# Performance work log

Hardware: AMD Instinct MI355X
Metric: run time of the kernel (lower is better)

## Reference

```python
import jax, jax.numpy as jnp
import numpy as np

B_SZ, SEQ_LEN, STATE_DIM, D_IN, D_OUT, KX = 8, 2048, 1024, 512, 512, 10


def setup_inputs() -> dict:
    key = jax.random.key(0)
    ks = jax.random.split(key, 7)
    inputs = jax.random.normal(ks[0], (B_SZ, SEQ_LEN, D_IN), dtype=jnp.float32)
    h0 = jax.random.normal(ks[1], (STATE_DIM,), dtype=jnp.float32)
    # exponential_decay_init(lam=15): x = clamp(-1/lam * log(1-u), max=1); A = (1-x)*sign
    u = jax.random.uniform(ks[2], (STATE_DIM,), dtype=jnp.float32)
    x = jnp.minimum(-(1.0 / 15.0) * jnp.log1p(-u), 1.0)
    sign = jnp.sign(jax.random.normal(ks[3], (STATE_DIM,), dtype=jnp.float32))
    A = (1.0 - x) * sign
    Bm = jax.random.normal(ks[4], (D_IN, STATE_DIM), dtype=jnp.float32) / D_IN
    C = jax.random.normal(ks[5], (STATE_DIM, D_OUT), dtype=jnp.float32) / STATE_DIM
    M = jax.random.normal(ks[6], (D_OUT, D_IN, KX), dtype=jnp.float32) / D_OUT
    return {"inputs": inputs, "h0": h0, "A": A, "B": Bm, "C": C, "M": M}


def _ar_preds(M, x):
    # Equivalent to einsum('oik,bli->bklo') + per-k roll + triu mask + sum over k:
    # ar[b,l,:] = sum_{i=0}^{k-1, i<=l} M[:,:,i] @ x[b, l-i, :]
    b, l, d_in = x.shape
    kx = M.shape[2]
    ar = jnp.einsum('oi,bli->blo', M[:, :, 0], x)
    for i in range(1, kx):
        x_shift = jnp.pad(x, ((0, 0), (i, 0), (0, 0)))[:, :l]  # shift right, zero-fill
        ar = ar + jnp.einsum('oi,bli->blo', M[:, :, i], x_shift)
    return ar


def reference(inputs, h0, A, B, C, M):
    b, l, d_in = inputs.shape
    state_dim = A.shape[0]
    # Project inputs once: u_t @ B for all t -> [b, l, s]
    uB = jnp.einsum('bli,is->bls', inputs, B)

    def step(h, u_t):
        h = A * h + u_t  # diagonal recurrence
        return h, h

    h_init = jnp.broadcast_to(h0, (b, state_dim))
    _, hs = jax.lax.scan(step, h_init, jnp.swapaxes(uB, 0, 1))  # [l, b, s]
    hs = jnp.swapaxes(hs, 0, 1)  # [b, l, s]
    lds_out = hs @ C  # [b, l, d_out]
    return lds_out + _ar_preds(M, inputs)
```

## Files before the change

kernel.cpp:

```cpp
#include <hip/hip_runtime.h>

#define B_SZ   8
#define SEQ    2048
#define PSEQ   (SEQ+16)
#define SDIM   1024
#define DIN    512
#define DOUT   512
#define KX     10
#define RTOT   (B_SZ*SEQ)
#define LC     64
#define NC     (SEQ/LC)

typedef __attribute__((ext_vector_type(8))) short short8;
typedef __attribute__((ext_vector_type(4))) float f32x4;
typedef __attribute__((ext_vector_type(4))) unsigned short bfx4;

#define OFF_XP   0UL
#define OFF_UB   16973824UL
#define OFF_HS   50528256UL
#define OFF_BT   84082688UL
#define OFF_CT   85131264UL
#define OFF_MT   86179840UL

__device__ __forceinline__ short f2bf(float f) {
  unsigned u = __builtin_bit_cast(unsigned, f);
  u += 0x7fffu + ((u >> 16) & 1u);
  return (short)(u >> 16);
}
__device__ __forceinline__ float bf2f(unsigned short b) {
  return __builtin_bit_cast(float, (unsigned)b << 16);
}

#define GLOAD16(gp, lp) __builtin_amdgcn_global_load_lds( \
    (const __attribute__((address_space(1))) void*)(gp), \
    (__attribute__((address_space(3))) void*)(lp), 16, 0, 0)
#define WAITVM(n) asm volatile("s_waitcnt vmcnt(" #n ")" ::: "memory")
#define LGKM0()   do { asm volatile("s_waitcnt lgkmcnt(0)" ::: "memory"); \
                       __builtin_amdgcn_sched_barrier(0); } while (0)
#define SBAR() __builtin_amdgcn_s_barrier()

__global__ void k_conv_x(const float* __restrict__ in, short* __restrict__ out) {
  const int NG = RTOT * (DIN / 8);
  for (int g = blockIdx.x * 256 + threadIdx.x; g < NG; g += 2048 * 256) {
    int r = g >> 6, c8 = g & 63;
    int b = r >> 11, t = r & 2047;
    const float4* p = reinterpret_cast<const float4*>(in) + (size_t)g * 2;
    float4 f0 = p[0], f1 = p[1];
    short8 o;
    o[0]=f2bf(f0.x); o[1]=f2bf(f0.y); o[2]=f2bf(f0.z); o[3]=f2bf(f0.w);
    o[4]=f2bf(f1.x); o[5]=f2bf(f1.y); o[6]=f2bf(f1.z); o[7]=f2bf(f1.w);
    *reinterpret_cast<short8*>(out + ((size_t)(b * PSEQ + 16 + t) * DIN + c8 * 8)) = o;
  }
}

__global__ void k_zero_pad(short* __restrict__ Xp) {
  int idx = blockIdx.x * 256 + threadIdx.x;
  if (idx >= B_SZ * 16 * (DIN / 8)) return;
  int b = idx >> 10, rem = idx & 1023;
  int row16 = rem >> 6, c8 = rem & 63;
  const short8 z = {0,0,0,0,0,0,0,0};
  *reinterpret_cast<short8*>(Xp + ((size_t)(b * PSEQ + row16) * DIN + c8 * 8)) = z;
}

__global__ void k_transpose_bf16(const float* __restrict__ in, short* __restrict__ out,
                                 int rows, int cols) {
  __shared__ float t[32][33];
  int bx = blockIdx.x * 32, by = blockIdx.y * 32;
  int tx = threadIdx.x & 31, ty = threadIdx.x >> 5;
  #pragma unroll
  for (int j = 0; j < 32; j += 8)
    t[ty + j][tx] = in[(size_t)(by + ty + j) * cols + (bx + tx)];
  __syncthreads();
  #pragma unroll
  for (int j = 0; j < 32; j += 8)
    out[(size_t)(bx + ty + j) * rows + (by + tx)] = f2bf(t[tx][ty + j]);
}

__global__ void k_prep_M(const float* __restrict__ M, short* __restrict__ Mt) {
  int idx = blockIdx.x * 256 + threadIdx.x;
  if (idx >= DOUT * DIN) return;
  int o = idx / DIN, i = idx - o * DIN;
  const float* src = M + ((size_t)o * DIN + i) * KX;
  #pragma unroll
  for (int t = 0; t < KX; ++t)
    Mt[((size_t)t * DOUT + o) * DIN + i] = f2bf(src[t]);
}

__global__ void k_scan_E(const short* __restrict__ uB, const float* __restrict__ A,
                         float* __restrict__ E) {
  int blk = blockIdx.x, tid = threadIdx.x;
  int b = blk >> 5, c = blk & 31;
  int s0 = tid * 4;
  const short* base = uB + ((size_t)b * SEQ + (size_t)c * LC) * SDIM + s0;
  float a[4], h[4];
  #pragma unroll
  for (int j = 0; j < 4; ++j) { a[j] = A[s0 + j]; h[j] = 0.f; }
  for (int t = 0; t < LC; ++t) {
    bfx4 v = *reinterpret_cast<const bfx4*>(base + (size_t)t * SDIM);
    #pragma unroll
    for (int j = 0; j < 4; ++j) h[j] = fmaf(a[j], h[j], bf2f(v[j]));
  }
  float* ep = E + (size_t)blk * SDIM + s0;
  #pragma unroll
  for (int j = 0; j < 4; ++j) ep[j] = h[j];
}

__global__ void k_scan_S(const float* __restrict__ E, const float* __restrict__ A,
                         const float* __restrict__ h0, float* __restrict__ Sb) {
  int blk = blockIdx.x, tid = threadIdx.x;
  int b = blk >> 2;
  int s = ((blk & 3) << 8) + tid;
  float a = A[s], ap = a;
  #pragma unroll
  for (int q = 0; q < 6; ++q) ap *= ap;
  float S = h0[s];
  for (int c = 0; c < NC; ++c) {
    size_t idx = ((size_t)b * NC + c) * SDIM + s;
    Sb[idx] = S;
    S = fmaf(ap, S, E[idx]);
  }
}

__global__ void k_scan_h(const short* __restrict__ uB, const float* __restrict__ A,
                         const float* __restrict__ Sb, short* __restrict__ hs) {
  int blk = blockIdx.x, tid = threadIdx.x;
  int b = blk >> 5, c = blk & 31;
  int s0 = tid * 4;
  const short* base = uB + ((size_t)b * SEQ + (size_t)c * LC) * SDIM + s0;
  short* hbase = hs + ((size_t)b * SEQ + (size_t)c * LC) * SDIM + s0;
  float a[4], h[4];
  #pragma unroll
  for (int j = 0; j < 4; ++j) {
    a[j] = A[s0 + j];
    h[j] = Sb[(size_t)blk * SDIM + s0 + j];
  }
  for (int t = 0; t < LC; ++t) {
    bfx4 v = *reinterpret_cast<const bfx4*>(base + (size_t)t * SDIM);
    bfx4 o;
    #pragma unroll
    for (int j = 0; j < 4; ++j) {
      h[j] = fmaf(a[j], h[j], bf2f(v[j]));
      o[j] = (unsigned short)f2bf(h[j]);
    }
    *reinterpret_cast<bfx4*>(hbase + (size_t)t * SDIM) = o;
  }
}

__device__ __forceinline__ void stage128(const short* __restrict__ g, int ld,
                                         short* l, int tid) {
  int rsub = tid >> 3;
  int slot = (tid & 7) ^ (rsub & 7);
  #pragma unroll
  for (int i = 0; i < 4; ++i) {
    int row = i * 32 + rsub;
    GLOAD16(g + (size_t)row * ld + slot * 8, l + row * 64 + (tid & 7) * 8);
  }
}

__device__ __forceinline__ void mfma_tile(const short* lA, int aoff, const short* lB,
                                          int lane, int wm, int wn, f32x4 acc[4][4]) {
  int lr = lane & 15;
  int h  = lane >> 4;
  #pragma unroll
  for (int kk = 0; kk < 2; ++kk) {
    int kslot = kk * 4 + h;
    short8 af[4], bfr[4];
    #pragma unroll
    for (int mi = 0; mi < 4; ++mi) {
      int row = aoff + wm * 64 + mi * 16 + lr;
      af[mi] = *reinterpret_cast<const short8*>(lA + row * 64 + ((kslot ^ (row & 7)) << 3));
    }
    #pragma unroll
    for (int ni = 0; ni < 4; ++ni) {
      int row = wn * 64 + ni * 16 + lr;
      bfr[ni] = *reinterpret_cast<const short8*>(lB + row * 64 + ((kslot ^ (row & 7)) << 3));
    }
    __builtin_amdgcn_s_setprio(1);
    #pragma unroll
    for (int mi = 0; mi < 4; ++mi)
      #pragma unroll
      for (int ni = 0; ni < 4; ++ni)
        acc[mi][ni] = __builtin_amdgcn_mfma_f32_16x16x32_bf16(af[mi], bfr[ni], acc[mi][ni], 0, 0, 0);
    __builtin_amdgcn_s_setprio(0);
  }
}

__global__ __launch_bounds__(256) void k_gemm_uB(const short* __restrict__ Xp,
                                                 const short* __restrict__ Bt,
                                                 short* __restrict__ uB) {
  __shared__ __attribute__((aligned(16))) short lds[32768];
  short* A0 = lds;         short* B0 = lds + 8192;
  short* A1 = lds + 16384; short* B1 = lds + 24576;
  int tid = threadIdx.x, lane = tid & 63, w = tid >> 6, wm = w >> 1, wn = w & 1;
  long r0 = (long)blockIdx.x * 128;
  int  c0 = blockIdx.y * 128;
  int  b  = (int)(r0 >> 11);
  const short* Abase = Xp + (size_t)(r0 + 16 * (b + 1)) * DIN;
  const short* Bbase = Bt + (size_t)c0 * DIN;
  const f32x4 z4 = {0.f, 0.f, 0.f, 0.f};
  f32x4 acc[4][4];
  #pragma unroll
  for (int mi = 0; mi < 4; ++mi)
    #pragma unroll
    for (int ni = 0; ni < 4; ++ni) acc[mi][ni] = z4;

  stage128(Abase, DIN, A0, tid);      stage128(Bbase, DIN, B0, tid);
  stage128(Abase + 64, DIN, A1, tid); stage128(Bbase + 64, DIN, B1, tid);
  WAITVM(8);
  SBAR();
  for (int kt = 0; kt < 8; ++kt) {
    const short* a  = (kt & 1) ? A1 : A0;
    const short* bb = (kt & 1) ? B1 : B0;
    mfma_tile(a, 0, bb, lane, wm, wn, acc);
    SBAR();
    if (kt + 2 < 8) {
      short* ad = (kt & 1) ? A1 : A0;
      short* bd = (kt & 1) ? B1 : B0;
      stage128(Abase + (kt + 2) * 64, DIN, ad, tid);
      stage128(Bbase + (kt + 2) * 64, DIN, bd, tid);
      WAITVM(8);
    } else {
      WAITVM(0);
    }
    SBAR();
  }
  #pragma unroll
  for (int mi = 0; mi < 4; ++mi)
    #pragma unroll
    for (int ni = 0; ni < 4; ++ni)
      #pragma unroll
      for (int r = 0; r < 4; ++r) {
        long row = r0 + wm * 64 + mi * 16 + (lane >> 4) * 4 + r;
        int  col = c0 + wn * 64 + ni * 16 + (lane & 15);
        uB[(size_t)row * SDIM + col] = f2bf(acc[mi][ni][r]);
      }
}


struct Frags { short8 a[4][2]; short8 b[4][2]; };

__device__ __forceinline__ void read_frags(Frags& f, const short* la, int aoff,
                                           const short* lb, int lane, int wm, int wn) {
  int lr = lane & 15, h = lane >> 4;
  #pragma unroll
  for (int kk = 0; kk < 2; ++kk) {
    int kslot = kk * 4 + h;
    #pragma unroll
    for (int mi = 0; mi < 4; ++mi) {
      int row = aoff + wm * 64 + mi * 16 + lr;
      f.a[mi][kk] = *reinterpret_cast<const short8*>(la + row * 64 + ((kslot ^ (row & 7)) << 3));
    }
    #pragma unroll
    for (int ni = 0; ni < 4; ++ni) {
      int row = wn * 64 + ni * 16 + lr;
      f.b[ni][kk] = *reinterpret_cast<const short8*>(lb + row * 64 + ((kslot ^ (row & 7)) << 3));
    }
  }
}

__device__ __forceinline__ void mfma_frags(const Frags& f, f32x4 acc[4][4]) {
  #pragma unroll
  for (int kk = 0; kk < 2; ++kk)
    #pragma unroll
    for (int mi = 0; mi < 4; ++mi)
      #pragma unroll
      for (int ni = 0; ni < 4; ++ni)
        acc[mi][ni] = __builtin_amdgcn_mfma_f32_16x16x32_bf16(f.a[mi][kk], f.b[ni][kk], acc[mi][ni], 0, 0, 0);
}

__device__ __forceinline__ void sgb_interleave() {
  #pragma unroll
  for (int i = 0; i < 16; ++i) {
    __builtin_amdgcn_sched_group_barrier(0x008, 2, 0);
    __builtin_amdgcn_sched_group_barrier(0x100, 1, 0);
  }
}

__device__ __forceinline__ void stageA256(const short* __restrict__ g, int ld,
                                          short* l, int tid) {
  int rsub = tid >> 3;
  int slot = (tid & 7) ^ (rsub & 7);
  #pragma unroll
  for (int i = 0; i < 4; ++i) {
    int row = i * 64 + rsub;
    GLOAD16(g + (size_t)row * ld + slot * 8, l + row * 64 + (tid & 7) * 8);
  }
}
__device__ __forceinline__ void stageB128(const short* __restrict__ g, int ld,
                                          short* l, int tid) {
  int rsub = tid >> 3;
  int slot = (tid & 7) ^ (rsub & 7);
  #pragma unroll
  for (int i = 0; i < 2; ++i) {
    int row = i * 64 + rsub;
    GLOAD16(g + (size_t)row * ld + slot * 8, l + row * 64 + (tid & 7) * 8);
  }
}
__device__ __forceinline__ void stageX320(const short* __restrict__ g,
                                          short* l, int tid) {
  int rsub = tid >> 3;
  int slot = (tid & 7) ^ (rsub & 7);
  #pragma unroll
  for (int i = 0; i < 5; ++i) {
    int row = i * 64 + rsub;
    GLOAD16(g + (size_t)row * DIN + slot * 8, l + row * 64 + (tid & 7) * 8);
  }
}

__global__ __launch_bounds__(512, 2) void k_gemm_out(const short* __restrict__ hs,
                                                     const short* __restrict__ Xp,
                                                     const short* __restrict__ Ct,
                                                     const short* __restrict__ Mt,
                                                     float* __restrict__ out) {
  __shared__ __attribute__((aligned(16))) short lds[81920];
  short* const P0  = lds;
  short* const P1  = lds + 24576;
  short* const P2  = lds + 49152;
  short* const Xs0 = lds;
  short* const Xs1 = lds + 20480;
  short* const PM0 = lds + 57344;
  short* const PM1 = lds + 65536;
  short* const PM2 = lds + 73728;
  int tid = threadIdx.x, lane = tid & 63, w = tid >> 6;
  int wm = w >> 1, wn = w & 1;
  int bid = blockIdx.x;
  int sw  = (bid & 7) * 32 + (bid >> 3);
  long r0 = (long)(sw & 63) * 256;
  int  c0 = (sw >> 6) * 128;
  int  b  = (int)(r0 >> 11);
  const short* hsA = hs + (size_t)r0 * SDIM;
  const short* CtB = Ct + (size_t)c0 * SDIM;
  const short* Xa  = Xp + (size_t)(r0 + 16 * (b + 1) - 16) * DIN;
  const short* MtB = Mt + (size_t)c0 * DIN;

  const f32x4 z4 = {0.f, 0.f, 0.f, 0.f};
  f32x4 acc[4][4];
  #pragma unroll
  for (int mi = 0; mi < 4; ++mi)
    #pragma unroll
    for (int ni = 0; ni < 4; ++ni) acc[mi][ni] = z4;

  Frags fr[2];

  stageA256(hsA,        SDIM, P0, tid);  stageB128(CtB,        SDIM, P0 + 16384, tid);
  stageA256(hsA + 64,   SDIM, P1, tid);  stageB128(CtB + 64,   SDIM, P1 + 16384, tid);
  stageA256(hsA + 128,  SDIM, P2, tid);  stageB128(CtB + 128,  SDIM, P2 + 16384, tid);
  WAITVM(6);
  SBAR();
  read_frags(fr[0], P0, 0, P0 + 16384, lane, wm, wn);

  #pragma unroll
  for (int s = 0; s < 16; ++s) {
    __builtin_amdgcn_s_setprio(1);
    mfma_frags(fr[s & 1], acc);
    if (s < 15) {
      const short* nb = ((s + 1) % 3 == 0) ? P0 : ((s + 1) % 3 == 1) ? P1 : P2;
      read_frags(fr[(s + 1) & 1], nb, 0, nb + 16384, lane, wm, wn);
    } else {
      read_frags(fr[0], Xs0, 16, PM0, lane, wm, wn);
    }
    sgb_interleave();
    __builtin_amdgcn_s_setprio(0);
    LGKM0();
    SBAR();
    if (s <= 12) {
      short* sp = (s % 3 == 0) ? P0 : (s % 3 == 1) ? P1 : P2;
      stageA256(hsA + (s + 3) * 64, SDIM, sp, tid);
      stageB128(CtB + (s + 3) * 64, SDIM, sp + 16384, tid);
      WAITVM(6);
    } else if (s == 13) {
      stageB128(MtB, DIN, PM0, tid);
      stageB128(MtB + (size_t)DOUT * DIN, DIN, PM1, tid);
      WAITVM(4);
    } else if (s == 14) {
      stageB128(MtB + (size_t)2 * DOUT * DIN, DIN, PM2, tid);
      stageX320(Xa, Xs0, tid);
      WAITVM(0);
    }
    SBAR();
  }

  for (int k0 = 0; k0 < 8; ++k0) {
    int kc = k0 * 64;
    const short* xs = (k0 & 1) ? Xs1 : Xs0;
    short*       xn = (k0 & 1) ? Xs0 : Xs1;
    const short* q0 = (k0 % 3 == 0) ? PM0 : (k0 % 3 == 1) ? PM1 : PM2;
    const short* q1 = (k0 % 3 == 0) ? PM1 : (k0 % 3 == 1) ? PM2 : PM0;
    const short* q2 = (k0 % 3 == 0) ? PM2 : (k0 % 3 == 1) ? PM0 : PM1;
    #pragma unroll
    for (int j = 0; j < KX; ++j) {
      __builtin_amdgcn_s_setprio(1);
      mfma_frags(fr[j & 1], acc);
      bool do_read = (j < 9) || (k0 < 7);
      if (j < 9) {
        const short* mn = ((j + 1) % 3 == 0) ? q0 : ((j + 1) % 3 == 1) ? q1 : q2;
        read_frags(fr[(j + 1) & 1], xs, 15 - j, mn, lane, wm, wn);
      } else if (k0 < 7) {
        read_frags(fr[0], xn, 16, q1, lane, wm, wn);
      }
      if (do_read) sgb_interleave();
      __builtin_amdgcn_s_setprio(0);
      LGKM0();
      SBAR();
      if (j + 3 <= 9) {
        short* mw = (j % 3 == 0) ? (short*)q0 : (j % 3 == 1) ? (short*)q1 : (short*)q2;
        stageB128(MtB + (size_t)(j + 3) * DOUT * DIN + kc, DIN, mw, tid);
      } else if (k0 < 7) {
        short* mw = (j % 3 == 0) ? (short*)q0 : (j % 3 == 1) ? (short*)q1 : (short*)q2;
        stageB128(MtB + (size_t)(j - 7) * DOUT * DIN + kc + 64, DIN, mw, tid);
      }
      if (j == 1 && k0 < 7) stageX320(Xa + kc + 64, xn, tid);
      if (j == 1 || j == 2) {
        if (k0 < 7) { WAITVM(7); } else { WAITVM(2); }
      } else if (j >= 7) {
        if (k0 == 7) { WAITVM(0); } else { WAITVM(2); }
      } else {
        WAITVM(2);
      }
      SBAR();
    }
  }

  #pragma unroll
  for (int mi = 0; mi < 4; ++mi)
    #pragma unroll
    for (int ni = 0; ni < 4; ++ni)
      #pragma unroll
      for (int r = 0; r < 4; ++r) {
        long row = r0 + wm * 64 + mi * 16 + (lane >> 4) * 4 + r;
        int  col = c0 + wn * 64 + ni * 16 + (lane & 15);
        out[(size_t)row * DOUT + col] = acc[mi][ni][r];
      }
}

extern "C" void kernel_launch(void* const* d_in, const int* in_sizes, int n_in,
                              void* d_out, int out_size, void* d_ws, size_t ws_size,
                              hipStream_t stream) {
  (void)in_sizes; (void)n_in; (void)out_size; (void)ws_size;
  const float* x  = (const float*)d_in[0];
  const float* h0 = (const float*)d_in[1];
  const float* A  = (const float*)d_in[2];
  const float* B  = (const float*)d_in[3];
  const float* C  = (const float*)d_in[4];
  const float* M  = (const float*)d_in[5];
  float* out = (float*)d_out;
  char* ws = (char*)d_ws;

  short* Xp  = (short*)(ws + OFF_XP);
  short* uB  = (short*)(ws + OFF_UB);
  short* hsb = (short*)(ws + OFF_HS);
  short* Bt  = (short*)(ws + OFF_BT);
  short* Ct  = (short*)(ws + OFF_CT);
  short* Mt  = (short*)(ws + OFF_MT);
  float* E   = out;
  float* Sb  = out + B_SZ * NC * SDIM;

  k_conv_x<<<2048, 256, 0, stream>>>(x, Xp);
  k_zero_pad<<<32, 256, 0, stream>>>(Xp);
  k_transpose_bf16<<<dim3(SDIM / 32, DIN / 32), 256, 0, stream>>>(B, Bt, DIN, SDIM);
  k_transpose_bf16<<<dim3(DOUT / 32, SDIM / 32), 256, 0, stream>>>(C, Ct, SDIM, DOUT);
  k_prep_M<<<(DOUT * DIN + 255) / 256, 256, 0, stream>>>(M, Mt);

  k_gemm_uB<<<dim3(RTOT / 128, SDIM / 128), 256, 0, stream>>>(Xp, Bt, uB);

  k_scan_E<<<B_SZ * NC, 256, 0, stream>>>(uB, A, E);
  k_scan_S<<<B_SZ * 4, 256, 0, stream>>>(E, A, h0, Sb);
  k_scan_h<<<B_SZ * NC, 256, 0, stream>>>(uB, A, Sb, hsb);

  k_gemm_out<<<256, 512, 0, stream>>>(hsb, Xp, Ct, Mt, out);
}
```

Before: 153.7 us.

## Fuse three scan kernels into one cooperative kernel with LDS-cached chunk

Replaces the three-pass chunked scan (local end states, carry propagation, final states) with one cooperative kernel that uses grid syncs between phases. Each block stages its 64x1024 bf16 uB chunk into shared memory once and reuses it for both passes, which avoids reading uB from global memory twice. Zero padding is also folded into the conversion kernel, removing a launch. The cost is two grid-wide barriers, 128KB of LDS per block, and a dependence on all 256 blocks being co-resident.

```diff
diff --git a/kernel.cpp b/kernel.cpp
--- a/kernel.cpp
+++ b/kernel.cpp
@@ -1,4 +1,7 @@
 #include <hip/hip_runtime.h>
+#include <hip/hip_cooperative_groups.h>
+
+namespace cg = cooperative_groups;
 
 #define B_SZ   8
 #define SEQ    2048
@@ -41,25 +44,25 @@
 
 __global__ void k_conv_x(const float* __restrict__ in, short* __restrict__ out) {
   const int NG = RTOT * (DIN / 8);
-  for (int g = blockIdx.x * 256 + threadIdx.x; g < NG; g += 2048 * 256) {
-    int r = g >> 6, c8 = g & 63;
-    int b = r >> 11, t = r & 2047;
-    const float4* p = reinterpret_cast<const float4*>(in) + (size_t)g * 2;
-    float4 f0 = p[0], f1 = p[1];
-    short8 o;
-    o[0]=f2bf(f0.x); o[1]=f2bf(f0.y); o[2]=f2bf(f0.z); o[3]=f2bf(f0.w);
-    o[4]=f2bf(f1.x); o[5]=f2bf(f1.y); o[6]=f2bf(f1.z); o[7]=f2bf(f1.w);
-    *reinterpret_cast<short8*>(out + ((size_t)(b * PSEQ + 16 + t) * DIN + c8 * 8)) = o;
-  }
-}
-
-__global__ void k_zero_pad(short* __restrict__ Xp) {
-  int idx = blockIdx.x * 256 + threadIdx.x;
-  if (idx >= B_SZ * 16 * (DIN / 8)) return;
-  int b = idx >> 10, rem = idx & 1023;
-  int row16 = rem >> 6, c8 = rem & 63;
-  const short8 z = {0,0,0,0,0,0,0,0};
-  *reinterpret_cast<short8*>(Xp + ((size_t)(b * PSEQ + row16) * DIN + c8 * 8)) = z;
+  const int NPAD = B_SZ * 16 * (DIN / 8);
+  for (int g = blockIdx.x * 256 + threadIdx.x; g < NG + NPAD; g += 2048 * 256) {
+    if (g < NG) {
+      int r = g >> 6, c8 = g & 63;
+      int b = r >> 11, t = r & 2047;
+      const float4* p = reinterpret_cast<const float4*>(in) + (size_t)g * 2;
+      float4 f0 = p[0], f1 = p[1];
+      short8 o;
+      o[0]=f2bf(f0.x); o[1]=f2bf(f0.y); o[2]=f2bf(f0.z); o[3]=f2bf(f0.w);
+      o[4]=f2bf(f1.x); o[5]=f2bf(f1.y); o[6]=f2bf(f1.z); o[7]=f2bf(f1.w);
+      *reinterpret_cast<short8*>(out + ((size_t)(b * PSEQ + 16 + t) * DIN + c8 * 8)) = o;
+    } else {
+      int idx = g - NG;
+      int b = idx >> 10, rem = idx & 1023;
+      int row16 = rem >> 6, c8 = rem & 63;
+      const short8 z = {0,0,0,0,0,0,0,0};
+      *reinterpret_cast<short8*>(out + ((size_t)(b * PSEQ + row16) * DIN + c8 * 8)) = z;
+    }
+  }
 }
 
 __global__ void k_transpose_bf16(const float* __restrict__ in, short* __restrict__ out,
@@ -86,63 +89,74 @@
     Mt[((size_t)t * DOUT + o) * DIN + i] = f2bf(src[t]);
 }
 
-__global__ void k_scan_E(const short* __restrict__ uB, const float* __restrict__ A,
-                         float* __restrict__ E) {
-  int blk = blockIdx.x, tid = threadIdx.x;
-  int b = blk >> 5, c = blk & 31;
+__global__ void __launch_bounds__(256) k_scan_all(const short* __restrict__ uB,
+                                                  const float* __restrict__ A,
+                                                  const float* __restrict__ h0,
+                                                  float* __restrict__ E,
+                                                  float* __restrict__ Sb,
+                                                  short* __restrict__ hs) {
+  __shared__ __attribute__((aligned(16))) short chunk[LC * SDIM];
+  cg::grid_group grid = cg::this_grid();
+  int g = blockIdx.x, tid = threadIdx.x;
+  int b = g >> 5, c = g & 31;
+  const short* src = uB + ((size_t)b * SEQ + (size_t)c * LC) * SDIM;
+
+  #pragma unroll
+  for (int i = 0; i < 32; ++i) {
+    int e8 = i * 256 + tid;
+    GLOAD16(src + e8 * 8, chunk + e8 * 8);
+  }
+  WAITVM(0);
+  SBAR();
+
   int s0 = tid * 4;
-  const short* base = uB + ((size_t)b * SEQ + (size_t)c * LC) * SDIM + s0;
-  float a[4], h[4];
-  #pragma unroll
-  for (int j = 0; j < 4; ++j) { a[j] = A[s0 + j]; h[j] = 0.f; }
-  for (int t = 0; t < LC; ++t) {
-    bfx4 v = *reinterpret_cast<const bfx4*>(base + (size_t)t * SDIM);
-    #pragma unroll
-    for (int j = 0; j < 4; ++j) h[j] = fmaf(a[j], h[j], bf2f(v[j]));
-  }
-  float* ep = E + (size_t)blk * SDIM + s0;
-  #pragma unroll
-  for (int j = 0; j < 4; ++j) ep[j] = h[j];
-}
-
-__global__ void k_scan_S(const float* __restrict__ E, const float* __restrict__ A,
-                         const float* __restrict__ h0, float* __restrict__ Sb) {
-  int blk = blockIdx.x, tid = threadIdx.x;
-  int b = blk >> 2;
-  int s = ((blk & 3) << 8) + tid;
-  float a = A[s], ap = a;
-  #pragma unroll
-  for (int q = 0; q < 6; ++q) ap *= ap;
-  float S = h0[s];
-  for (int c = 0; c < NC; ++c) {
-    size_t idx = ((size_t)b * NC + c) * SDIM + s;
-    Sb[idx] = S;
-    S = fmaf(ap, S, E[idx]);
-  }
-}
-
-__global__ void k_scan_h(const short* __restrict__ uB, const float* __restrict__ A,
-                         const float* __restrict__ Sb, short* __restrict__ hs) {
-  int blk = blockIdx.x, tid = threadIdx.x;
-  int b = blk >> 5, c = blk & 31;
-  int s0 = tid * 4;
-  const short* base = uB + ((size_t)b * SEQ + (size_t)c * LC) * SDIM + s0;
-  short* hbase = hs + ((size_t)b * SEQ + (size_t)c * LC) * SDIM + s0;
-  float a[4], h[4];
-  #pragma unroll
-  for (int j = 0; j < 4; ++j) {
-    a[j] = A[s0 + j];
-    h[j] = Sb[(size_t)blk * SDIM + s0 + j];
-  }
-  for (int t = 0; t < LC; ++t) {
-    bfx4 v = *reinterpret_cast<const bfx4*>(base + (size_t)t * SDIM);
-    bfx4 o;
-    #pragma unroll
-    for (int j = 0; j < 4; ++j) {
-      h[j] = fmaf(a[j], h[j], bf2f(v[j]));
-      o[j] = (unsigned short)f2bf(h[j]);
-    }
-    *reinterpret_cast<bfx4*>(hbase + (size_t)t * SDIM) = o;
+  float a0 = A[s0], a1 = A[s0+1], a2 = A[s0+2], a3 = A[s0+3];
+  {
+    float e0 = 0.f, e1 = 0.f, e2 = 0.f, e3 = 0.f;
+    for (int t = 0; t < LC; ++t) {
+      bfx4 v = *reinterpret_cast<const bfx4*>(chunk + t * SDIM + s0);
+      e0 = fmaf(a0, e0, bf2f(v[0]));
+      e1 = fmaf(a1, e1, bf2f(v[1]));
+      e2 = fmaf(a2, e2, bf2f(v[2]));
+      e3 = fmaf(a3, e3, bf2f(v[3]));
+    }
+    float4 ev = { e0, e1, e2, e3 };
+    *reinterpret_cast<float4*>(E + (size_t)g * SDIM + s0) = ev;
+  }
+  grid.sync();
+
+  if (g < 32) {
+    int bb = g >> 2;
+    int s = ((g & 3) << 8) + tid;
+    float a = A[s], ap = a;
+    #pragma unroll
+    for (int q = 0; q < 6; ++q) ap *= ap;
+    float S = h0[s];
+    for (int c2 = 0; c2 < NC; ++c2) {
+      size_t idx = ((size_t)bb * NC + c2) * SDIM + s;
+      Sb[idx] = S;
+      S = fmaf(ap, S, E[idx]);
+    }
+  }
+  grid.sync();
+
+  {
+    float4 sv = *reinterpret_cast<const float4*>(Sb + (size_t)g * SDIM + s0);
+    float h0_ = sv.x, h1_ = sv.y, h2_ = sv.z, h3_ = sv.w;
+    short* dst = hs + ((size_t)b * SEQ + (size_t)c * LC) * SDIM + s0;
+    for (int t = 0; t < LC; ++t) {
+      bfx4 v = *reinterpret_cast<const bfx4*>(chunk + t * SDIM + s0);
+      h0_ = fmaf(a0, h0_, bf2f(v[0]));
+      h1_ = fmaf(a1, h1_, bf2f(v[1]));
+      h2_ = fmaf(a2, h2_, bf2f(v[2]));
+      h3_ = fmaf(a3, h3_, bf2f(v[3]));
+      bfx4 o;
+      o[0] = (unsigned short)f2bf(h0_);
+      o[1] = (unsigned short)f2bf(h1_);
+      o[2] = (unsigned short)f2bf(h2_);
+      o[3] = (unsigned short)f2bf(h3_);
+      *reinterpret_cast<bfx4*>(dst + (size_t)t * SDIM) = o;
+    }
   }
 }
 
@@ -235,7 +249,6 @@
         uB[(size_t)row * SDIM + col] = f2bf(acc[mi][ni][r]);
       }
 }
-
 
 struct Frags { short8 a[4][2]; short8 b[4][2]; };
 
@@ -456,16 +469,18 @@
   float* Sb  = out + B_SZ * NC * SDIM;
 
   k_conv_x<<<2048, 256, 0, stream>>>(x, Xp);
-  k_zero_pad<<<32, 256, 0, stream>>>(Xp);
   k_transpose_bf16<<<dim3(SDIM / 32, DIN / 32), 256, 0, stream>>>(B, Bt, DIN, SDIM);
   k_transpose_bf16<<<dim3(DOUT / 32, SDIM / 32), 256, 0, stream>>>(C, Ct, SDIM, DOUT);
   k_prep_M<<<(DOUT * DIN + 255) / 256, 256, 0, stream>>>(M, Mt);
 
   k_gemm_uB<<<dim3(RTOT / 128, SDIM / 128), 256, 0, stream>>>(Xp, Bt, uB);
 
-  k_scan_E<<<B_SZ * NC, 256, 0, stream>>>(uB, A, E);
-  k_scan_S<<<B_SZ * 4, 256, 0, stream>>>(E, A, h0, Sb);
-  k_scan_h<<<B_SZ * NC, 256, 0, stream>>>(uB, A, Sb, hsb);
+  {
+    void* args[] = { (void*)&uB, (void*)&A, (void*)&h0,
+                     (void*)&E, (void*)&Sb, (void*)&hsb };
+    hipLaunchCooperativeKernel(reinterpret_cast<void*>(k_scan_all),
+                               dim3(256), dim3(256), args, 0, stream);
+  }
 
   k_gemm_out<<<256, 512, 0, stream>>>(hsb, Xp, Ct, Mt, out);
 }
```

Result: slower. 214.6 us (+39.6%).

## Fuse prep kernels into one launch and fold chunk-carry scan into scan_h

Applied to the files above, without the earlier changes.

Merges the five preprocessing kernels (x conversion, zero pad, B/C transposes, M repack) into a single kernel whose block index picks the task, which removes four launches and lets the pieces overlap. It also drops the separate carry-propagation kernel. Each k_scan_h block instead recomputes its own starting state by serially folding all earlier chunk end-states, so there are fewer launches and no Sb round trip. The cost is redundant work that grows with chunk index: up to 31 extra float4 loads and FMAs per thread. Dispatch in the prep kernel also diverges by block.

```diff
diff --git a/kernel.cpp b/kernel.cpp
--- a/kernel.cpp
+++ b/kernel.cpp
@@ -39,34 +39,12 @@
                        __builtin_amdgcn_sched_barrier(0); } while (0)
 #define SBAR() __builtin_amdgcn_s_barrier()
 
-__global__ void k_conv_x(const float* __restrict__ in, short* __restrict__ out) {
-  const int NG = RTOT * (DIN / 8);
-  for (int g = blockIdx.x * 256 + threadIdx.x; g < NG; g += 2048 * 256) {
-    int r = g >> 6, c8 = g & 63;
-    int b = r >> 11, t = r & 2047;
-    const float4* p = reinterpret_cast<const float4*>(in) + (size_t)g * 2;
-    float4 f0 = p[0], f1 = p[1];
-    short8 o;
-    o[0]=f2bf(f0.x); o[1]=f2bf(f0.y); o[2]=f2bf(f0.z); o[3]=f2bf(f0.w);
-    o[4]=f2bf(f1.x); o[5]=f2bf(f1.y); o[6]=f2bf(f1.z); o[7]=f2bf(f1.w);
-    *reinterpret_cast<short8*>(out + ((size_t)(b * PSEQ + 16 + t) * DIN + c8 * 8)) = o;
-  }
-}
-
-__global__ void k_zero_pad(short* __restrict__ Xp) {
-  int idx = blockIdx.x * 256 + threadIdx.x;
-  if (idx >= B_SZ * 16 * (DIN / 8)) return;
-  int b = idx >> 10, rem = idx & 1023;
-  int row16 = rem >> 6, c8 = rem & 63;
-  const short8 z = {0,0,0,0,0,0,0,0};
-  *reinterpret_cast<short8*>(Xp + ((size_t)(b * PSEQ + row16) * DIN + c8 * 8)) = z;
-}
-
-__global__ void k_transpose_bf16(const float* __restrict__ in, short* __restrict__ out,
-                                 int rows, int cols) {
-  __shared__ float t[32][33];
-  int bx = blockIdx.x * 32, by = blockIdx.y * 32;
-  int tx = threadIdx.x & 31, ty = threadIdx.x >> 5;
+__device__ __forceinline__ void transpose_tile(const float* __restrict__ in,
+                                               short* __restrict__ out,
+                                               int rows, int cols, int bxi, int byi,
+                                               int tid, float (*t)[33]) {
+  int bx = bxi * 32, by = byi * 32;
+  int tx = tid & 31, ty = tid >> 5;
   #pragma unroll
   for (int j = 0; j < 32; j += 8)
     t[ty + j][tx] = in[(size_t)(by + ty + j) * cols + (bx + tx)];
@@ -76,14 +54,49 @@
     out[(size_t)(bx + ty + j) * rows + (by + tx)] = f2bf(t[tx][ty + j]);
 }
 
-__global__ void k_prep_M(const float* __restrict__ M, short* __restrict__ Mt) {
-  int idx = blockIdx.x * 256 + threadIdx.x;
-  if (idx >= DOUT * DIN) return;
-  int o = idx / DIN, i = idx - o * DIN;
-  const float* src = M + ((size_t)o * DIN + i) * KX;
-  #pragma unroll
-  for (int t = 0; t < KX; ++t)
-    Mt[((size_t)t * DOUT + o) * DIN + i] = f2bf(src[t]);
+__global__ void k_prep(const float* __restrict__ x,  const float* __restrict__ B,
+                       const float* __restrict__ C,  const float* __restrict__ M,
+                       short* __restrict__ Xp, short* __restrict__ Bt,
+                       short* __restrict__ Ct, short* __restrict__ Mt) {
+  __shared__ float t[32][33];
+  int blk = blockIdx.x, tid = threadIdx.x;
+  if (blk < 2048) {
+    const int NG = RTOT * (DIN / 8);
+    const int NPAD = B_SZ * 16 * (DIN / 8);
+    for (int g = blk * 256 + tid; g < NG + NPAD; g += 2048 * 256) {
+      if (g < NG) {
+        int r = g >> 6, c8 = g & 63;
+        int b = r >> 11, tt = r & 2047;
+        const float4* p = reinterpret_cast<const float4*>(x) + (size_t)g * 2;
+        float4 f0 = p[0], f1 = p[1];
+        short8 o;
+        o[0]=f2bf(f0.x); o[1]=f2bf(f0.y); o[2]=f2bf(f0.z); o[3]=f2bf(f0.w);
+        o[4]=f2bf(f1.x); o[5]=f2bf(f1.y); o[6]=f2bf(f1.z); o[7]=f2bf(f1.w);
+        *reinterpret_cast<short8*>(Xp + ((size_t)(b * PSEQ + 16 + tt) * DIN + c8 * 8)) = o;
+      } else {
+        int idx = g - NG;
+        int b = idx >> 10, rem = idx & 1023;
+        int row16 = rem >> 6, c8 = rem & 63;
+        const short8 z = {0,0,0,0,0,0,0,0};
+        *reinterpret_cast<short8*>(Xp + ((size_t)(b * PSEQ + row16) * DIN + c8 * 8)) = z;
+      }
+    }
+  } else if (blk < 2560) {
+    int idx = blk - 2048;
+    transpose_tile(B, Bt, DIN, SDIM, idx & 31, idx >> 5, tid, t);
+  } else if (blk < 3072) {
+    int idx = blk - 2560;
+    transpose_tile(C, Ct, SDIM, DOUT, idx & 15, idx >> 4, tid, t);
+  } else {
+    int idx = (blk - 3072) * 256 + tid;
+    if (idx < DOUT * DIN) {
+      int o = idx / DIN, i = idx - o * DIN;
+      const float* src = M + ((size_t)o * DIN + i) * KX;
+      #pragma unroll
+      for (int tt = 0; tt < KX; ++tt)
+        Mt[((size_t)tt * DOUT + o) * DIN + i] = f2bf(src[tt]);
+    }
+  }
 }
 
 __global__ void k_scan_E(const short* __restrict__ uB, const float* __restrict__ A,
@@ -105,35 +118,32 @@
   for (int j = 0; j < 4; ++j) ep[j] = h[j];
 }
 
-__global__ void k_scan_S(const float* __restrict__ E, const float* __restrict__ A,
-                         const float* __restrict__ h0, float* __restrict__ Sb) {
-  int blk = blockIdx.x, tid = threadIdx.x;
-  int b = blk >> 2;
-  int s = ((blk & 3) << 8) + tid;
-  float a = A[s], ap = a;
-  #pragma unroll
-  for (int q = 0; q < 6; ++q) ap *= ap;
-  float S = h0[s];
-  for (int c = 0; c < NC; ++c) {
-    size_t idx = ((size_t)b * NC + c) * SDIM + s;
-    Sb[idx] = S;
-    S = fmaf(ap, S, E[idx]);
-  }
-}
-
 __global__ void k_scan_h(const short* __restrict__ uB, const float* __restrict__ A,
-                         const float* __restrict__ Sb, short* __restrict__ hs) {
+                         const float* __restrict__ h0, const float* __restrict__ E,
+                         short* __restrict__ hs) {
   int blk = blockIdx.x, tid = threadIdx.x;
   int b = blk >> 5, c = blk & 31;
   int s0 = tid * 4;
+  float a[4], h[4], ap[4];
+  #pragma unroll
+  for (int j = 0; j < 4; ++j) {
+    a[j] = A[s0 + j];
+    float p = a[j];
+    #pragma unroll
+    for (int q = 0; q < 6; ++q) p *= p;
+    ap[j] = p;
+    h[j] = h0[s0 + j];
+  }
+  const float* Eb = E + (size_t)b * NC * SDIM + s0;
+  for (int c2 = 0; c2 < c; ++c2) {
+    float4 ev = *reinterpret_cast<const float4*>(Eb + (size_t)c2 * SDIM);
+    h[0] = fmaf(ap[0], h[0], ev.x);
+    h[1] = fmaf(ap[1], h[1], ev.y);
+    h[2] = fmaf(ap[2], h[2], ev.z);
+    h[3] = fmaf(ap[3], h[3], ev.w);
+  }
   const short* base = uB + ((size_t)b * SEQ + (size_t)c * LC) * SDIM + s0;
   short* hbase = hs + ((size_t)b * SEQ + (size_t)c * LC) * SDIM + s0;
-  float a[4], h[4];
-  #pragma unroll
-  for (int j = 0; j < 4; ++j) {
-    a[j] = A[s0 + j];
-    h[j] = Sb[(size_t)blk * SDIM + s0 + j];
-  }
   for (int t = 0; t < LC; ++t) {
     bfx4 v = *reinterpret_cast<const bfx4*>(base + (size_t)t * SDIM);
     bfx4 o;
@@ -235,7 +245,6 @@
         uB[(size_t)row * SDIM + col] = f2bf(acc[mi][ni][r]);
       }
 }
-
 
 struct Frags { short8 a[4][2]; short8 b[4][2]; };
 
@@ -453,19 +462,10 @@
   short* Ct  = (short*)(ws + OFF_CT);
   short* Mt  = (short*)(ws + OFF_MT);
   float* E   = out;
-  float* Sb  = out + B_SZ * NC * SDIM;
-
-  k_conv_x<<<2048, 256, 0, stream>>>(x, Xp);
-  k_zero_pad<<<32, 256, 0, stream>>>(Xp);
-  k_transpose_bf16<<<dim3(SDIM / 32, DIN / 32), 256, 0, stream>>>(B, Bt, DIN, SDIM);
-  k_transpose_bf16<<<dim3(DOUT / 32, SDIM / 32), 256, 0, stream>>>(C, Ct, SDIM, DOUT);
-  k_prep_M<<<(DOUT * DIN + 255) / 256, 256, 0, stream>>>(M, Mt);
-
+
+  k_prep<<<4096, 256, 0, stream>>>(x, B, C, M, Xp, Bt, Ct, Mt);
   k_gemm_uB<<<dim3(RTOT / 128, SDIM / 128), 256, 0, stream>>>(Xp, Bt, uB);
-
   k_scan_E<<<B_SZ * NC, 256, 0, stream>>>(uB, A, E);
-  k_scan_S<<<B_SZ * 4, 256, 0, stream>>>(E, A, h0, Sb);
-  k_scan_h<<<B_SZ * NC, 256, 0, stream>>>(uB, A, Sb, hsb);
-
+  k_scan_h<<<B_SZ * NC, 256, 0, stream>>>(uB, A, h0, E, hsb);
   k_gemm_out<<<256, 512, 0, stream>>>(hsb, Xp, Ct, Mt, out);
 }
```

After: 151.8 us. About the same (-1.2%).
